# Kernel optimization log

Measured on AMD Instinct MI355X. Metric: run time of the kernel, lower is better.

The kernel has to match this reference:

```python
import jax, jax.numpy as jnp
import numpy as np

B, IN, HID, OUT, E = 8192, 1024, 4096, 1024, 8
EPS = 1e-5  # torch LayerNorm default


def _layernorm(x, gamma, beta):
    # normalize over last axis; gamma/beta broadcast as [E, dim] against [B, E, dim]
    mu = jnp.mean(x, axis=-1, keepdims=True)
    var = jnp.var(x, axis=-1, keepdims=True)
    return (x - mu) * jax.lax.rsqrt(var + EPS) * gamma + beta


def setup_inputs() -> dict:
    key = jax.random.key(0)
    ks = jax.random.split(key, 8)
    x = jax.random.normal(ks[0], (B, IN), dtype=jnp.float32)
    weights = jax.random.uniform(ks[1], (B, E), dtype=jnp.float32)
    s1 = 1.0 / np.sqrt(IN)
    s2 = 1.0 / np.sqrt(HID)
    W1 = jax.random.uniform(ks[2], (E, IN, HID), minval=-s1, maxval=s1, dtype=jnp.float32)
    b1 = jax.random.uniform(ks[3], (E, HID), minval=-s1, maxval=s1, dtype=jnp.float32)
    W2 = jax.random.uniform(ks[4], (E, HID, OUT), minval=-s2, maxval=s2, dtype=jnp.float32)
    b2 = jax.random.uniform(ks[5], (E, OUT), minval=-s2, maxval=s2, dtype=jnp.float32)
    g1 = jnp.ones((E, HID), dtype=jnp.float32)
    be1 = jnp.zeros((E, HID), dtype=jnp.float32)
    g2 = jnp.ones((E, OUT), dtype=jnp.float32)
    be2 = jnp.zeros((E, OUT), dtype=jnp.float32)
    return {"x": x, "weights": weights, "W1": W1, "b1": b1, "g1": g1, "be1": be1,
            "W2": W2, "b2": b2, "g2": g2, "be2": be2}


def reference(x, weights, W1, b1, g1, be1, W2, b2, g2, be2):
    # Each expert MLP([1024,4096,1024]): Linear -> LN -> GELU -> Linear -> LN -> GELU
    # (MLP appends LayerNorm + activation after EVERY Linear, including the last).
    # Dropout p=0 / eval mode -> identity. All experts run on every token.
    h = jnp.einsum('bi,eih->beh', x, W1) + b1          # [B, E, HID]
    h = jax.nn.gelu(_layernorm(h, g1, be1), approximate=False)
    y = jnp.einsum('beh,eho->beo', h, W2) + b2         # [B, E, OUT]
    y = jax.nn.gelu(_layernorm(y, g2, be2), approximate=False)
    # weighted combine: einsum('bij,bi->bj')
    return jnp.einsum('beo,be->bo', y, weights)        # [B, OUT]
```

## Files before the change

### kernel.cpp

```cpp
#include <hip/hip_runtime.h>
#include <cstdint>
#include <cstddef>

typedef unsigned short u16;
typedef float f32x4 __attribute__((ext_vector_type(4)));
typedef __bf16 bf16x8 __attribute__((ext_vector_type(8)));

#define B_DIM   8192
#define IN_DIM  1024
#define HID_DIM 4096
#define OUT_DIM 1024
#define NEXP    8

__device__ __forceinline__ u16 f2b(float f) {
    uint32_t u = __builtin_bit_cast(uint32_t, f);
    u += 0x7fffu + ((u >> 16) & 1u);
    return (u16)(u >> 16);
}
__device__ __forceinline__ float b2f(u16 b) {
    uint32_t u = ((uint32_t)b) << 16;
    return __builtin_bit_cast(float, u);
}
__device__ __forceinline__ float gelu_fast(float x) {
    float y = x * (0.7978845608f + 0.03567740814f * x * x);
    float a = fminf(y * 2.8853900818f, 80.0f);
    float e = __builtin_amdgcn_exp2f(a);
    return x * e * __builtin_amdgcn_rcpf(e + 1.0f);
}
__device__ __forceinline__ void async_cp16(const void* g, void* l) {
    __builtin_amdgcn_global_load_lds(
        (const __attribute__((address_space(1))) void*)g,
        (__attribute__((address_space(3))) void*)l,
        16, 0, 0);
}

__global__ __launch_bounds__(256)
void cvt_bf16(const float* __restrict__ in, u16* __restrict__ out, int n4) {
    int i = blockIdx.x * 256 + threadIdx.x;
    if (i >= n4) return;
    float4 v = *(const float4*)&in[(size_t)i * 4];
    uint2 o;
    o.x = (uint32_t)f2b(v.x) | ((uint32_t)f2b(v.y) << 16);
    o.y = (uint32_t)f2b(v.z) | ((uint32_t)f2b(v.w) << 16);
    *(uint2*)&out[(size_t)i * 4] = o;
}

__global__ __launch_bounds__(256)
void transpose_cvt2(const float* __restrict__ W1e, u16* __restrict__ w1t,
                    const float* __restrict__ W2e, u16* __restrict__ w2t) {
    __shared__ float tile[32][33];
    const float* W; u16* Wt; int K, N, n0, k0;
    if (blockIdx.z == 0) {
        W = W1e; Wt = w1t; K = IN_DIM; N = HID_DIM;
        n0 = blockIdx.x * 32; k0 = blockIdx.y * 32;
    } else {
        W = W2e; Wt = w2t; K = HID_DIM; N = OUT_DIM;
        n0 = blockIdx.y * 32; k0 = blockIdx.x * 32;
    }
    const int tx = threadIdx.x & 31, ty = threadIdx.x >> 5;
#pragma unroll
    for (int i = 0; i < 4; ++i) {
        int k = k0 + ty + i * 8;
        tile[ty + i * 8][tx] = W[(size_t)k * N + n0 + tx];
    }
    __syncthreads();
#pragma unroll
    for (int i = 0; i < 4; ++i) {
        int n = n0 + ty + i * 8;
        Wt[(size_t)n * K + k0 + tx] = f2b(tile[tx][ty + i * 8]);
    }
}

template<int F32OUT>
__global__ __launch_bounds__(512, 2)
void gemm256_8ph(const u16* __restrict__ A, const u16* __restrict__ Bt,
                 const float* __restrict__ bias, void* __restrict__ Cv,
                 int M, int N, int lda, int ldb, int Ksl) {
    __shared__ __attribute__((aligned(16))) u16 sA[32768];
    __shared__ __attribute__((aligned(16))) u16 sB[32768];

    const int tid  = threadIdx.x;
    const int wid  = tid >> 6;
    const int lane = tid & 63;
    const int quad = lane >> 4;
    const int lr   = lane & 15;
    const int wm   = wid >> 2;
    const int wn   = wid & 3;
    const int z    = blockIdx.z;

    const int NX = gridDim.x, NY = gridDim.y;
    const int bid = blockIdx.y * NX + blockIdx.x;
    const int xcd = bid & 7;
    const int j   = bid >> 3;
    const int yl  = j / NX;
    const int bx  = j - yl * NX;
    const int by  = xcd * (NY >> 3) + yl;
    const int m0 = by * 256;
    const int n0 = bx * 256;

    const int qsw   = (lr >> 1) & 3;
    const int row_s = tid >> 2;
    const int lc    = ((tid & 3) ^ ((tid >> 3) & 3)) * 8;

    const u16* Ast = A  + (size_t)z * Ksl + (size_t)(m0 + row_s) * lda + lc;
    const u16* Bst = Bt + (size_t)z * Ksl + (size_t)(n0 + row_s) * ldb + lc;

    const int rdA = (wm * 128 + lr) * 32 + ((quad ^ qsw) * 8);
    const int rdB = (wn * 64  + lr) * 32 + ((quad ^ qsw) * 8);
    const int d0  = tid * 8;

    const int NT = Ksl >> 6;

    f32x4 acc[8][4] = {};
    bf16x8 av[4], bv[4];

#define STG_A(hb, ko) do {                                                     \
        async_cp16(Ast + (ko),                      &sA[(hb) + d0]);           \
        async_cp16(Ast + (ko) + (size_t)128 * lda,  &sA[(hb) + d0 + 4096]);    \
    } while (0)
#define STG_B(hb, ko) do {                                                     \
        async_cp16(Bst + (ko),                      &sB[(hb) + d0]);           \
        async_cp16(Bst + (ko) + (size_t)128 * ldb,  &sB[(hb) + d0 + 4096]);    \
    } while (0)
#define RD_A4(hb, MO) do { _Pragma("unroll")                                   \
        for (int mi_ = 0; mi_ < 4; ++mi_)                                      \
            av[mi_] = *(const bf16x8*)&sA[(hb) + rdA + ((MO) + mi_) * 512];    \
    } while (0)
#define RD_B4(hb) do { _Pragma("unroll")                                       \
        for (int ni_ = 0; ni_ < 4; ++ni_)                                      \
            bv[ni_] = *(const bf16x8*)&sB[(hb) + rdB + ni_ * 512];             \
    } while (0)
#define SYNC_MFMA16(MO) do {                                                   \
        __builtin_amdgcn_s_barrier();                                          \
        asm volatile("s_waitcnt lgkmcnt(0)");                                  \
        __builtin_amdgcn_sched_barrier(0);                                     \
        __builtin_amdgcn_s_setprio(1);                                         \
        _Pragma("unroll")                                                      \
        for (int mi_ = 0; mi_ < 4; ++mi_)                                      \
            _Pragma("unroll")                                                  \
            for (int ni_ = 0; ni_ < 4; ++ni_)                                  \
                acc[(MO) + mi_][ni_] = __builtin_amdgcn_mfma_f32_16x16x32_bf16(\
                    av[mi_], bv[ni_], acc[(MO) + mi_][ni_], 0, 0, 0);          \
        __builtin_amdgcn_s_setprio(0);                                         \
    } while (0)

    STG_A(0, 0);      STG_B(0, 0);
    STG_A(8192, 32);  STG_B(8192, 32);
    asm volatile("s_waitcnt vmcnt(4)");
    __builtin_amdgcn_s_barrier();

#pragma unroll 1
    for (int t = 0; t < NT - 1; ++t) {
        const int cb = (t & 1) << 14;
        const int nb = cb ^ 16384;
        const size_t kt = (size_t)(t + 1) * 64;
        RD_A4(cb, 0); RD_B4(cb);
        STG_A(nb, kt);
        SYNC_MFMA16(0);
        __builtin_amdgcn_s_barrier();
        RD_A4(cb, 4);
        STG_B(nb, kt);
        SYNC_MFMA16(4);
        asm volatile("s_waitcnt vmcnt(4)");
        __builtin_amdgcn_s_barrier();
        RD_A4(cb + 8192, 0); RD_B4(cb + 8192);
        STG_A(nb + 8192, kt + 32);
        SYNC_MFMA16(0);
        __builtin_amdgcn_s_barrier();
        RD_A4(cb + 8192, 4);
        STG_B(nb + 8192, kt + 32);
        SYNC_MFMA16(4);
        asm volatile("s_waitcnt vmcnt(4)");
        __builtin_amdgcn_s_barrier();
    }
    {
        const int cb = ((NT - 1) & 1) << 14;
        RD_A4(cb, 0); RD_B4(cb);
        SYNC_MFMA16(0);
        __builtin_amdgcn_s_barrier();
        RD_A4(cb, 4);
        SYNC_MFMA16(4);
        asm volatile("s_waitcnt vmcnt(0)");
        __builtin_amdgcn_s_barrier();
        RD_A4(cb + 8192, 0); RD_B4(cb + 8192);
        SYNC_MFMA16(0);
        __builtin_amdgcn_s_barrier();
        RD_A4(cb + 8192, 4);
        SYNC_MFMA16(4);
    }
#undef SYNC_MFMA16
#undef RD_B4
#undef RD_A4
#undef STG_B
#undef STG_A

    if constexpr (F32OUT) {
        float* C = (float*)Cv + (size_t)z * ((size_t)M * N);
#pragma unroll
        for (int mi = 0; mi < 8; ++mi) {
            const int mr = m0 + wm * 128 + mi * 16 + quad * 4;
#pragma unroll
            for (int r = 0; r < 4; ++r) {
                float* Crow = C + (size_t)(mr + r) * N + n0 + wn * 64 + lr;
#pragma unroll
                for (int ni = 0; ni < 4; ++ni)
                    Crow[ni * 16] = acc[mi][ni][r];
            }
        }
    } else {
        u16* C = (u16*)Cv;
        float bvv[4];
#pragma unroll
        for (int ni = 0; ni < 4; ++ni)
            bvv[ni] = bias[n0 + wn * 64 + ni * 16 + lr];
#pragma unroll
        for (int mi = 0; mi < 8; ++mi) {
            const int mr = m0 + wm * 128 + mi * 16 + quad * 4;
#pragma unroll
            for (int r = 0; r < 4; ++r) {
                u16* Crow = C + (size_t)(mr + r) * N + n0 + wn * 64 + lr;
#pragma unroll
                for (int ni = 0; ni < 4; ++ni)
                    Crow[ni * 16] = f2b(acc[mi][ni][r] + bvv[ni]);
            }
        }
    }
}

__global__ __launch_bounds__(256)
void gemm_bt_bias(const u16* __restrict__ A, const u16* __restrict__ Bt,
                  const float* __restrict__ bias, u16* __restrict__ C,
                  int M, int N, int K) {
    __shared__ __attribute__((aligned(16))) u16 sA[2][128 * 32];
    __shared__ __attribute__((aligned(16))) u16 sB[2][128 * 32];

    const int tid  = threadIdx.x;
    const int wid  = tid >> 6;
    const int lane = tid & 63;
    const int quad = lane >> 4;
    const int lr   = lane & 15;
    const int wm   = wid & 1;
    const int wn   = wid >> 1;

    const int NX = gridDim.x, NY = gridDim.y;
    const int bid = blockIdx.y * NX + blockIdx.x;
    const int xcd = bid & 7;
    const int j   = bid >> 3;
    const int yl  = j / NX;
    const int bx  = j - yl * NX;
    const int by  = xcd * (NY >> 3) + yl;

    const int m0 = by * 128;
    const int n0 = bx * 128;

    const int sr  = lane >> 2;
    const int scl = ((lane & 3) ^ ((lane >> 3) & 3)) * 8;
    const int qsw = (lr >> 1) & 3;

    const u16* Ag = A + (size_t)m0 * K;
    const u16* Bg = Bt + (size_t)n0 * K;

    f32x4 acc[4][4] = {};

    for (int k0 = 0; k0 < K; k0 += 64) {
#pragma unroll
        for (int s = 0; s < 2; ++s) {
#pragma unroll
            for (int i = 0; i < 2; ++i) {
                const int rb = wid * 32 + i * 16;
                async_cp16(Ag + (size_t)(rb + sr) * K + k0 + s * 32 + scl,
                           &sA[s][rb * 32]);
                async_cp16(Bg + (size_t)(rb + sr) * K + k0 + s * 32 + scl,
                           &sB[s][rb * 32]);
            }
        }
        __syncthreads();

#pragma unroll
        for (int s = 0; s < 2; ++s) {
            bf16x8 af[4], bfr[4];
#pragma unroll
            for (int mi = 0; mi < 4; ++mi)
                af[mi] = *(const bf16x8*)
                    &sA[s][(wm * 64 + mi * 16 + lr) * 32 + ((quad ^ qsw) * 8)];
#pragma unroll
            for (int ni = 0; ni < 4; ++ni)
                bfr[ni] = *(const bf16x8*)
                    &sB[s][(wn * 64 + ni * 16 + lr) * 32 + ((quad ^ qsw) * 8)];

#pragma unroll
            for (int mi = 0; mi < 4; ++mi)
#pragma unroll
                for (int ni = 0; ni < 4; ++ni)
                    acc[mi][ni] = __builtin_amdgcn_mfma_f32_16x16x32_bf16(
                        af[mi], bfr[ni], acc[mi][ni], 0, 0, 0);
        }

        __syncthreads();
    }

    float bvv[4];
#pragma unroll
    for (int ni = 0; ni < 4; ++ni)
        bvv[ni] = bias[n0 + wn * 64 + ni * 16 + lr];

#pragma unroll
    for (int mi = 0; mi < 4; ++mi) {
        const int mr = m0 + wm * 64 + mi * 16 + quad * 4;
#pragma unroll
        for (int r = 0; r < 4; ++r) {
            u16* Crow = C + (size_t)(mr + r) * N + n0 + wn * 64 + lr;
#pragma unroll
            for (int ni = 0; ni < 4; ++ni)
                Crow[ni * 16] = f2b(acc[mi][ni][r] + bvv[ni]);
        }
    }
}

__global__ __launch_bounds__(256)
void ln_gelu_hid(u16* __restrict__ h, const float* __restrict__ g,
                 const float* __restrict__ be) {
    __shared__ float red[8];
    const int row = blockIdx.x;
    u16* hp = h + (size_t)row * HID_DIM;
    const int t = threadIdx.x;

    uint4 v0 = *(const uint4*)&hp[t * 8];
    uint4 v1 = *(const uint4*)&hp[(t + 256) * 8];

    float vals[16];
    {
        const uint32_t w0[4] = {v0.x, v0.y, v0.z, v0.w};
        const uint32_t w1[4] = {v1.x, v1.y, v1.z, v1.w};
#pragma unroll
        for (int q = 0; q < 4; ++q) {
            vals[q * 2]     = b2f((u16)(w0[q] & 0xffffu));
            vals[q * 2 + 1] = b2f((u16)(w0[q] >> 16));
            vals[8 + q * 2]     = b2f((u16)(w1[q] & 0xffffu));
            vals[8 + q * 2 + 1] = b2f((u16)(w1[q] >> 16));
        }
    }
    float s = 0.f, ss = 0.f;
#pragma unroll
    for (int i = 0; i < 16; ++i) { s += vals[i]; ss += vals[i] * vals[i]; }

    float4 gv[4], bv[4];
    gv[0] = *(const float4*)&g[t * 8];
    gv[1] = *(const float4*)&g[t * 8 + 4];
    gv[2] = *(const float4*)&g[(t + 256) * 8];
    gv[3] = *(const float4*)&g[(t + 256) * 8 + 4];
    bv[0] = *(const float4*)&be[t * 8];
    bv[1] = *(const float4*)&be[t * 8 + 4];
    bv[2] = *(const float4*)&be[(t + 256) * 8];
    bv[3] = *(const float4*)&be[(t + 256) * 8 + 4];

#pragma unroll
    for (int off = 32; off > 0; off >>= 1) {
        s += __shfl_down(s, off, 64);
        ss += __shfl_down(ss, off, 64);
    }
    if ((t & 63) == 0) { red[(t >> 6) * 2] = s; red[(t >> 6) * 2 + 1] = ss; }
    __syncthreads();
    s  = red[0] + red[2] + red[4] + red[6];
    ss = red[1] + red[3] + red[5] + red[7];
    const float mean = s * (1.f / HID_DIM);
    const float rstd = rsqrtf(ss * (1.f / HID_DIM) - mean * mean + 1e-5f);

    const float* gf = (const float*)gv;
    const float* bf = (const float*)bv;
#pragma unroll
    for (int j = 0; j < 2; ++j) {
        uint4 o;
        uint32_t* ow = (uint32_t*)&o;
#pragma unroll
        for (int q = 0; q < 4; ++q) {
            const int k = j * 8 + q * 2;
            float u0 = gelu_fast((vals[k]     - mean) * rstd * gf[k]     + bf[k]);
            float u1 = gelu_fast((vals[k + 1] - mean) * rstd * gf[k + 1] + bf[k + 1]);
            ow[q] = (uint32_t)f2b(u0) | ((uint32_t)f2b(u1) << 16);
        }
        *(uint4*)&hp[(t + j * 256) * 8] = o;
    }
}

__global__ __launch_bounds__(256)
void ln_gelu_combine(const u16* __restrict__ y, const float* __restrict__ g,
                     const float* __restrict__ be, const float* __restrict__ wts,
                     float* __restrict__ out, int e, int first) {
    __shared__ float red[8];
    const int row = blockIdx.x;
    const u16* yp = y + (size_t)row * OUT_DIM;
    const int t = threadIdx.x;

    uint2 v = *(const uint2*)&yp[t * 4];
    float f0 = b2f((u16)(v.x & 0xffffu)), f1 = b2f((u16)(v.x >> 16));
    float f2 = b2f((u16)(v.y & 0xffffu)), f3 = b2f((u16)(v.y >> 16));
    float s = f0 + f1 + f2 + f3;
    float ss = f0 * f0 + f1 * f1 + f2 * f2 + f3 * f3;

    const int n = t * 4;
    float4 gv = *(const float4*)&g[n];
    float4 bvv = *(const float4*)&be[n];

#pragma unroll
    for (int off = 32; off > 0; off >>= 1) {
        s += __shfl_down(s, off, 64);
        ss += __shfl_down(ss, off, 64);
    }
    if ((t & 63) == 0) { red[(t >> 6) * 2] = s; red[(t >> 6) * 2 + 1] = ss; }
    __syncthreads();
    s  = red[0] + red[2] + red[4] + red[6];
    ss = red[1] + red[3] + red[5] + red[7];
    const float mean = s * (1.f / OUT_DIM);
    const float rstd = rsqrtf(ss * (1.f / OUT_DIM) - mean * mean + 1e-5f);

    const float w = wts[(size_t)row * NEXP + e];
    float4 o;
    if (first) { o.x = o.y = o.z = o.w = 0.f; }
    else       { o = *(const float4*)&out[(size_t)row * OUT_DIM + n]; }
    o.x += w * gelu_fast((f0 - mean) * rstd * gv.x + bvv.x);
    o.y += w * gelu_fast((f1 - mean) * rstd * gv.y + bvv.y);
    o.z += w * gelu_fast((f2 - mean) * rstd * gv.z + bvv.z);
    o.w += w * gelu_fast((f3 - mean) * rstd * gv.w + bvv.w);
    *(float4*)&out[(size_t)row * OUT_DIM + n] = o;
}

__global__ __launch_bounds__(256)
void ln_gelu_combine_f32(const float* __restrict__ P, const float* __restrict__ g,
                         const float* __restrict__ be, const float* __restrict__ bs,
                         const float* __restrict__ wts, float* __restrict__ out,
                         int e, int first) {
    __shared__ float red[8];
    const int row = blockIdx.x;
    const int t = threadIdx.x;
    const int n = t * 4;

    const float* p0 = P + (size_t)row * OUT_DIM + n;
    const float* p1 = p0 + (size_t)B_DIM * OUT_DIM;
    float4 a  = *(const float4*)p0;
    float4 b  = *(const float4*)p1;
    float4 c  = *(const float4*)&bs[n];
    float f0 = a.x + b.x + c.x, f1 = a.y + b.y + c.y;
    float f2 = a.z + b.z + c.z, f3 = a.w + b.w + c.w;
    float s = f0 + f1 + f2 + f3;
    float ss = f0 * f0 + f1 * f1 + f2 * f2 + f3 * f3;

    float4 gv = *(const float4*)&g[n];
    float4 bvv = *(const float4*)&be[n];

#pragma unroll
    for (int off = 32; off > 0; off >>= 1) {
        s += __shfl_down(s, off, 64);
        ss += __shfl_down(ss, off, 64);
    }
    if ((t & 63) == 0) { red[(t >> 6) * 2] = s; red[(t >> 6) * 2 + 1] = ss; }
    __syncthreads();
    s  = red[0] + red[2] + red[4] + red[6];
    ss = red[1] + red[3] + red[5] + red[7];
    const float mean = s * (1.f / OUT_DIM);
    const float rstd = rsqrtf(ss * (1.f / OUT_DIM) - mean * mean + 1e-5f);

    const float w = wts[(size_t)row * NEXP + e];
    float4 o;
    if (first) { o.x = o.y = o.z = o.w = 0.f; }
    else       { o = *(const float4*)&out[(size_t)row * OUT_DIM + n]; }
    o.x += w * gelu_fast((f0 - mean) * rstd * gv.x + bvv.x);
    o.y += w * gelu_fast((f1 - mean) * rstd * gv.y + bvv.y);
    o.z += w * gelu_fast((f2 - mean) * rstd * gv.z + bvv.z);
    o.w += w * gelu_fast((f3 - mean) * rstd * gv.w + bvv.w);
    *(float4*)&out[(size_t)row * OUT_DIM + n] = o;
}

extern "C" void kernel_launch(void* const* d_in, const int* in_sizes, int n_in,
                              void* d_out, int out_size, void* d_ws, size_t ws_size,
                              hipStream_t stream) {
    (void)in_sizes; (void)n_in; (void)out_size;
    const float* x   = (const float*)d_in[0];
    const float* wts = (const float*)d_in[1];
    const float* W1  = (const float*)d_in[2];
    const float* b1  = (const float*)d_in[3];
    const float* g1  = (const float*)d_in[4];
    const float* be1 = (const float*)d_in[5];
    const float* W2  = (const float*)d_in[6];
    const float* b2  = (const float*)d_in[7];
    const float* g2  = (const float*)d_in[8];
    const float* be2 = (const float*)d_in[9];
    float* out = (float*)d_out;

    char* p = (char*)d_ws;
    u16* xb  = (u16*)p; p += (size_t)B_DIM * IN_DIM * 2;
    u16* w1t = (u16*)p; p += (size_t)HID_DIM * IN_DIM * 2;
    u16* w2t = (u16*)p; p += (size_t)OUT_DIM * HID_DIM * 2;
    u16* h   = (u16*)p; p += (size_t)B_DIM * HID_DIM * 2;
    float* P = (float*)p;
    u16*  y  = (u16*)p;

    const size_t need = (size_t)B_DIM * IN_DIM * 2 + (size_t)HID_DIM * IN_DIM * 2 +
                        (size_t)OUT_DIM * HID_DIM * 2 + (size_t)B_DIM * HID_DIM * 2 +
                        (size_t)2 * B_DIM * OUT_DIM * 4;
    const int splitk = (ws_size >= need) ? 1 : 0;

    cvt_bf16<<<(B_DIM * IN_DIM / 4 + 255) / 256, 256, 0, stream>>>(x, xb, B_DIM * IN_DIM / 4);

    for (int e = 0; e < NEXP; ++e) {
        transpose_cvt2<<<dim3(HID_DIM / 32, IN_DIM / 32, 2), 256, 0, stream>>>(
            W1 + (size_t)e * IN_DIM * HID_DIM, w1t,
            W2 + (size_t)e * HID_DIM * OUT_DIM, w2t);
        gemm256_8ph<0><<<dim3(HID_DIM / 256, B_DIM / 256, 1), 512, 0, stream>>>(
            xb, w1t, b1 + (size_t)e * HID_DIM, h, B_DIM, HID_DIM, IN_DIM, IN_DIM, IN_DIM);
        ln_gelu_hid<<<B_DIM, 256, 0, stream>>>(h, g1 + (size_t)e * HID_DIM,
                                               be1 + (size_t)e * HID_DIM);
        if (splitk) {
            gemm256_8ph<1><<<dim3(OUT_DIM / 256, B_DIM / 256, 2), 512, 0, stream>>>(
                h, w2t, nullptr, P, B_DIM, OUT_DIM, HID_DIM, HID_DIM, HID_DIM / 2);
            ln_gelu_combine_f32<<<B_DIM, 256, 0, stream>>>(
                P, g2 + (size_t)e * OUT_DIM, be2 + (size_t)e * OUT_DIM,
                b2 + (size_t)e * OUT_DIM, wts, out, e, e == 0 ? 1 : 0);
        } else {
            gemm_bt_bias<<<dim3(OUT_DIM / 128, B_DIM / 128), 256, 0, stream>>>(
                h, w2t, b2 + (size_t)e * OUT_DIM, y, B_DIM, OUT_DIM, HID_DIM);
            ln_gelu_combine<<<B_DIM, 256, 0, stream>>>(y, g2 + (size_t)e * OUT_DIM,
                                                       be2 + (size_t)e * OUT_DIM, wts, out,
                                                       e, e == 0 ? 1 : 0);
        }
    }
}
```

Baseline: 1.862 ms.

## Switch GEMM to 32x32x16 MFMA and store split-K partials as bf16

The GEMM inner loop now uses 32x32x16 bf16 MFMA instructions with 4x2 f32x16 accumulators instead of 16x16x32, and the LDS read indexing is changed to match the new operand layout. The aim is fewer MFMA issues and better operand reuse per LDS read. The split-K partial outputs are also written as bf16 instead of f32, which halves partial traffic and the workspace requirement. The cost is lost precision, since partial sums are rounded to bf16 before they are combined.

```diff
diff --git a/kernel.cpp b/kernel.cpp
--- a/kernel.cpp
+++ b/kernel.cpp
@@ -4,6 +4,7 @@
 
 typedef unsigned short u16;
 typedef float f32x4 __attribute__((ext_vector_type(4)));
+typedef float f32x16 __attribute__((ext_vector_type(16)));
 typedef __bf16 bf16x8 __attribute__((ext_vector_type(8)));
 
 #define B_DIM   8192
@@ -71,10 +72,10 @@
     }
 }
 
-template<int F32OUT>
+template<int PARTIAL>
 __global__ __launch_bounds__(512, 2)
 void gemm256_8ph(const u16* __restrict__ A, const u16* __restrict__ Bt,
-                 const float* __restrict__ bias, void* __restrict__ Cv,
+                 const float* __restrict__ bias, u16* __restrict__ C,
                  int M, int N, int lda, int ldb, int Ksl) {
     __shared__ __attribute__((aligned(16))) u16 sA[32768];
     __shared__ __attribute__((aligned(16))) u16 sB[32768];
@@ -82,8 +83,8 @@
     const int tid  = threadIdx.x;
     const int wid  = tid >> 6;
     const int lane = tid & 63;
-    const int quad = lane >> 4;
-    const int lr   = lane & 15;
+    const int l31  = lane & 31;
+    const int hi   = lane >> 5;
     const int wm   = wid >> 2;
     const int wn   = wid & 3;
     const int z    = blockIdx.z;
@@ -98,20 +99,22 @@
     const int m0 = by * 256;
     const int n0 = bx * 256;
 
-    const int qsw   = (lr >> 1) & 3;
+    const int xk    = (lane >> 1) & 3;
     const int row_s = tid >> 2;
     const int lc    = ((tid & 3) ^ ((tid >> 3) & 3)) * 8;
 
     const u16* Ast = A  + (size_t)z * Ksl + (size_t)(m0 + row_s) * lda + lc;
     const u16* Bst = Bt + (size_t)z * Ksl + (size_t)(n0 + row_s) * ldb + lc;
 
-    const int rdA = (wm * 128 + lr) * 32 + ((quad ^ qsw) * 8);
-    const int rdB = (wn * 64  + lr) * 32 + ((quad ^ qsw) * 8);
+    const int rdA = (wm * 128 + l31) * 32;
+    const int rdB = (wn * 64  + l31) * 32;
+    const int ck0 = ((0 + hi) ^ xk) * 8;
+    const int ck1 = ((2 + hi) ^ xk) * 8;
     const int d0  = tid * 8;
 
     const int NT = Ksl >> 6;
 
-    f32x4 acc[8][4] = {};
+    f32x16 acc[4][2] = {};
     bf16x8 av[4], bv[4];
 
 #define STG_A(hb, ko) do {                                                     \
@@ -122,25 +125,31 @@
         async_cp16(Bst + (ko),                      &sB[(hb) + d0]);           \
         async_cp16(Bst + (ko) + (size_t)128 * ldb,  &sB[(hb) + d0 + 4096]);    \
     } while (0)
-#define RD_A4(hb, MO) do { _Pragma("unroll")                                   \
-        for (int mi_ = 0; mi_ < 4; ++mi_)                                      \
-            av[mi_] = *(const bf16x8*)&sA[(hb) + rdA + ((MO) + mi_) * 512];    \
+#define RD_A4(hb, MF0) do {                                                    \
+        av[0] = *(const bf16x8*)&sA[(hb) + rdA + (MF0) * 1024 + ck0];          \
+        av[1] = *(const bf16x8*)&sA[(hb) + rdA + (MF0) * 1024 + ck1];          \
+        av[2] = *(const bf16x8*)&sA[(hb) + rdA + ((MF0) + 1) * 1024 + ck0];    \
+        av[3] = *(const bf16x8*)&sA[(hb) + rdA + ((MF0) + 1) * 1024 + ck1];    \
     } while (0)
-#define RD_B4(hb) do { _Pragma("unroll")                                       \
-        for (int ni_ = 0; ni_ < 4; ++ni_)                                      \
-            bv[ni_] = *(const bf16x8*)&sB[(hb) + rdB + ni_ * 512];             \
+#define RD_B4(hb) do {                                                         \
+        bv[0] = *(const bf16x8*)&sB[(hb) + rdB + ck0];                         \
+        bv[1] = *(const bf16x8*)&sB[(hb) + rdB + ck1];                         \
+        bv[2] = *(const bf16x8*)&sB[(hb) + rdB + 1024 + ck0];                  \
+        bv[3] = *(const bf16x8*)&sB[(hb) + rdB + 1024 + ck1];                  \
     } while (0)
-#define SYNC_MFMA16(MO) do {                                                   \
+#define CLUSTER8(A0) do {                                                      \
         __builtin_amdgcn_s_barrier();                                          \
         asm volatile("s_waitcnt lgkmcnt(0)");                                  \
         __builtin_amdgcn_sched_barrier(0);                                     \
         __builtin_amdgcn_s_setprio(1);                                         \
-        _Pragma("unroll")                                                      \
-        for (int mi_ = 0; mi_ < 4; ++mi_)                                      \
-            _Pragma("unroll")                                                  \
-            for (int ni_ = 0; ni_ < 4; ++ni_)                                  \
-                acc[(MO) + mi_][ni_] = __builtin_amdgcn_mfma_f32_16x16x32_bf16(\
-                    av[mi_], bv[ni_], acc[(MO) + mi_][ni_], 0, 0, 0);          \
+        acc[(A0)][0]     = __builtin_amdgcn_mfma_f32_32x32x16_bf16(av[0], bv[0], acc[(A0)][0],     0, 0, 0); \
+        acc[(A0)][1]     = __builtin_amdgcn_mfma_f32_32x32x16_bf16(av[0], bv[2], acc[(A0)][1],     0, 0, 0); \
+        acc[(A0) + 1][0] = __builtin_amdgcn_mfma_f32_32x32x16_bf16(av[2], bv[0], acc[(A0) + 1][0], 0, 0, 0); \
+        acc[(A0) + 1][1] = __builtin_amdgcn_mfma_f32_32x32x16_bf16(av[2], bv[2], acc[(A0) + 1][1], 0, 0, 0); \
+        acc[(A0)][0]     = __builtin_amdgcn_mfma_f32_32x32x16_bf16(av[1], bv[1], acc[(A0)][0],     0, 0, 0); \
+        acc[(A0)][1]     = __builtin_amdgcn_mfma_f32_32x32x16_bf16(av[1], bv[3], acc[(A0)][1],     0, 0, 0); \
+        acc[(A0) + 1][0] = __builtin_amdgcn_mfma_f32_32x32x16_bf16(av[3], bv[1], acc[(A0) + 1][0], 0, 0, 0); \
+        acc[(A0) + 1][1] = __builtin_amdgcn_mfma_f32_32x32x16_bf16(av[3], bv[3], acc[(A0) + 1][1], 0, 0, 0); \
         __builtin_amdgcn_s_setprio(0);                                         \
     } while (0)
 
@@ -156,72 +165,71 @@
         const size_t kt = (size_t)(t + 1) * 64;
         RD_A4(cb, 0); RD_B4(cb);
         STG_A(nb, kt);
-        SYNC_MFMA16(0);
-        __builtin_amdgcn_s_barrier();
-        RD_A4(cb, 4);
+        CLUSTER8(0);
+        __builtin_amdgcn_s_barrier();
+        RD_A4(cb, 2);
         STG_B(nb, kt);
-        SYNC_MFMA16(4);
+        CLUSTER8(2);
         asm volatile("s_waitcnt vmcnt(4)");
         __builtin_amdgcn_s_barrier();
         RD_A4(cb + 8192, 0); RD_B4(cb + 8192);
         STG_A(nb + 8192, kt + 32);
-        SYNC_MFMA16(0);
-        __builtin_amdgcn_s_barrier();
-        RD_A4(cb + 8192, 4);
+        CLUSTER8(0);
+        __builtin_amdgcn_s_barrier();
+        RD_A4(cb + 8192, 2);
         STG_B(nb + 8192, kt + 32);
-        SYNC_MFMA16(4);
+        CLUSTER8(2);
         asm volatile("s_waitcnt vmcnt(4)");
         __builtin_amdgcn_s_barrier();
     }
     {
         const int cb = ((NT - 1) & 1) << 14;
         RD_A4(cb, 0); RD_B4(cb);
-        SYNC_MFMA16(0);
-        __builtin_amdgcn_s_barrier();
-        RD_A4(cb, 4);
-        SYNC_MFMA16(4);
+        CLUSTER8(0);
+        __builtin_amdgcn_s_barrier();
+        RD_A4(cb, 2);
+        CLUSTER8(2);
         asm volatile("s_waitcnt vmcnt(0)");
         __builtin_amdgcn_s_barrier();
         RD_A4(cb + 8192, 0); RD_B4(cb + 8192);
-        SYNC_MFMA16(0);
-        __builtin_amdgcn_s_barrier();
-        RD_A4(cb + 8192, 4);
-        SYNC_MFMA16(4);
-    }
-#undef SYNC_MFMA16
+        CLUSTER8(0);
+        __builtin_amdgcn_s_barrier();
+        RD_A4(cb + 8192, 2);
+        CLUSTER8(2);
+    }
+#undef CLUSTER8
 #undef RD_B4
 #undef RD_A4
 #undef STG_B
 #undef STG_A
 
-    if constexpr (F32OUT) {
-        float* C = (float*)Cv + (size_t)z * ((size_t)M * N);
-#pragma unroll
-        for (int mi = 0; mi < 8; ++mi) {
-            const int mr = m0 + wm * 128 + mi * 16 + quad * 4;
-#pragma unroll
-            for (int r = 0; r < 4; ++r) {
-                float* Crow = C + (size_t)(mr + r) * N + n0 + wn * 64 + lr;
-#pragma unroll
-                for (int ni = 0; ni < 4; ++ni)
-                    Crow[ni * 16] = acc[mi][ni][r];
+    if constexpr (PARTIAL) {
+        u16* Cb = C + (size_t)z * ((size_t)M * N);
+#pragma unroll
+        for (int mf = 0; mf < 4; ++mf) {
+            const int mb = m0 + wm * 128 + mf * 32 + hi * 4;
+#pragma unroll
+            for (int rq = 0; rq < 4; ++rq)
+#pragma unroll
+            for (int rr = 0; rr < 4; ++rr) {
+                u16* Crow = Cb + (size_t)(mb + rr + rq * 8) * N + n0 + wn * 64 + l31;
+                Crow[0]  = f2b(acc[mf][0][rq * 4 + rr]);
+                Crow[32] = f2b(acc[mf][1][rq * 4 + rr]);
             }
         }
     } else {
-        u16* C = (u16*)Cv;
-        float bvv[4];
-#pragma unroll
-        for (int ni = 0; ni < 4; ++ni)
-            bvv[ni] = bias[n0 + wn * 64 + ni * 16 + lr];
-#pragma unroll
-        for (int mi = 0; mi < 8; ++mi) {
-            const int mr = m0 + wm * 128 + mi * 16 + quad * 4;
-#pragma unroll
-            for (int r = 0; r < 4; ++r) {
-                u16* Crow = C + (size_t)(mr + r) * N + n0 + wn * 64 + lr;
-#pragma unroll
-                for (int ni = 0; ni < 4; ++ni)
-                    Crow[ni * 16] = f2b(acc[mi][ni][r] + bvv[ni]);
+        const float bv0 = bias[n0 + wn * 64 + l31];
+        const float bv1 = bias[n0 + wn * 64 + 32 + l31];
+#pragma unroll
+        for (int mf = 0; mf < 4; ++mf) {
+            const int mb = m0 + wm * 128 + mf * 32 + hi * 4;
+#pragma unroll
+            for (int rq = 0; rq < 4; ++rq)
+#pragma unroll
+            for (int rr = 0; rr < 4; ++rr) {
+                u16* Crow = C + (size_t)(mb + rr + rq * 8) * N + n0 + wn * 64 + l31;
+                Crow[0]  = f2b(acc[mf][0][rq * 4 + rr] + bv0);
+                Crow[32] = f2b(acc[mf][1][rq * 4 + rr] + bv1);
             }
         }
     }
@@ -426,7 +434,7 @@
 }
 
 __global__ __launch_bounds__(256)
-void ln_gelu_combine_f32(const float* __restrict__ P, const float* __restrict__ g,
+void ln_gelu_combine_2bf(const u16* __restrict__ P, const float* __restrict__ g,
                          const float* __restrict__ be, const float* __restrict__ bs,
                          const float* __restrict__ wts, float* __restrict__ out,
                          int e, int first) {
@@ -435,13 +443,15 @@
     const int t = threadIdx.x;
     const int n = t * 4;
 
-    const float* p0 = P + (size_t)row * OUT_DIM + n;
-    const float* p1 = p0 + (size_t)B_DIM * OUT_DIM;
-    float4 a  = *(const float4*)p0;
-    float4 b  = *(const float4*)p1;
+    const u16* p0 = P + (size_t)row * OUT_DIM + n;
+    const u16* p1 = p0 + (size_t)B_DIM * OUT_DIM;
+    uint2 a = *(const uint2*)p0;
+    uint2 b = *(const uint2*)p1;
     float4 c  = *(const float4*)&bs[n];
-    float f0 = a.x + b.x + c.x, f1 = a.y + b.y + c.y;
-    float f2 = a.z + b.z + c.z, f3 = a.w + b.w + c.w;
+    float f0 = b2f((u16)(a.x & 0xffffu)) + b2f((u16)(b.x & 0xffffu)) + c.x;
+    float f1 = b2f((u16)(a.x >> 16))     + b2f((u16)(b.x >> 16))     + c.y;
+    float f2 = b2f((u16)(a.y & 0xffffu)) + b2f((u16)(b.y & 0xffffu)) + c.z;
+    float f3 = b2f((u16)(a.y >> 16))     + b2f((u16)(b.y >> 16))     + c.w;
     float s = f0 + f1 + f2 + f3;
     float ss = f0 * f0 + f1 * f1 + f2 * f2 + f3 * f3;
 
@@ -492,12 +502,12 @@
     u16* w1t = (u16*)p; p += (size_t)HID_DIM * IN_DIM * 2;
     u16* w2t = (u16*)p; p += (size_t)OUT_DIM * HID_DIM * 2;
     u16* h   = (u16*)p; p += (size_t)B_DIM * HID_DIM * 2;
-    float* P = (float*)p;
-    u16*  y  = (u16*)p;
+    u16* P   = (u16*)p;
+    u16* y   = (u16*)p;
 
     const size_t need = (size_t)B_DIM * IN_DIM * 2 + (size_t)HID_DIM * IN_DIM * 2 +
                         (size_t)OUT_DIM * HID_DIM * 2 + (size_t)B_DIM * HID_DIM * 2 +
-                        (size_t)2 * B_DIM * OUT_DIM * 4;
+                        (size_t)2 * B_DIM * OUT_DIM * 2;
     const int splitk = (ws_size >= need) ? 1 : 0;
 
     cvt_bf16<<<(B_DIM * IN_DIM / 4 + 255) / 256, 256, 0, stream>>>(x, xb, B_DIM * IN_DIM / 4);
@@ -513,7 +523,7 @@
         if (splitk) {
             gemm256_8ph<1><<<dim3(OUT_DIM / 256, B_DIM / 256, 2), 512, 0, stream>>>(
                 h, w2t, nullptr, P, B_DIM, OUT_DIM, HID_DIM, HID_DIM, HID_DIM / 2);
-            ln_gelu_combine_f32<<<B_DIM, 256, 0, stream>>>(
+            ln_gelu_combine_2bf<<<B_DIM, 256, 0, stream>>>(
                 P, g2 + (size_t)e * OUT_DIM, be2 + (size_t)e * OUT_DIM,
                 b2 + (size_t)e * OUT_DIM, wts, out, e, e == 0 ? 1 : 0);
         } else {
```

Result: slower. 1.910 ms (+2.6%).

## Use 256x512 triple-buffered GEMM for layer 1 and bf16 split-K partials

Applied to the files above, without the earlier changes.

Adds a new 1024-thread GEMM kernel with a 256x512 output tile and three-stage async LDS buffering for the first expert linear layer. The larger tile raises arithmetic intensity and halves the block count. The split-K second GEMM now writes its partial sums as bf16 instead of fp32, and the combine kernel reads bf16, which halves partial-sum traffic. The trade-off is one block per CU, higher register and LDS pressure, and extra rounding in the partial sums.

```diff
diff --git a/kernel.cpp b/kernel.cpp
--- a/kernel.cpp
+++ b/kernel.cpp
@@ -71,11 +71,135 @@
     }
 }
 
-template<int F32OUT>
+__global__ __launch_bounds__(1024, 1)
+void gemm256x512_bt(const u16* __restrict__ A, const u16* __restrict__ Bt,
+                    const float* __restrict__ bias, u16* __restrict__ C,
+                    int M, int N, int lda, int ldb, int K) {
+    __shared__ __attribute__((aligned(16))) u16 sA[3 * 8192];
+    __shared__ __attribute__((aligned(16))) u16 sB[3 * 16384];
+
+    const int tid  = threadIdx.x;
+    const int wid  = tid >> 6;
+    const int lane = tid & 63;
+    const int quad = lane >> 4;
+    const int lr   = lane & 15;
+    const int wm   = wid >> 3;
+    const int wn   = wid & 7;
+
+    const int NX = gridDim.x, NY = gridDim.y;
+    const int bid = blockIdx.y * NX + blockIdx.x;
+    const int xcd = bid & 7;
+    const int j   = bid >> 3;
+    const int yl  = j / NX;
+    const int bx  = j - yl * NX;
+    const int by  = xcd * (NY >> 3) + yl;
+    const int m0 = by * 256;
+    const int n0 = bx * 512;
+
+    const int qsw   = (lr >> 1) & 3;
+    const int row_s = tid >> 2;
+    const int lc    = ((tid & 3) ^ ((tid >> 3) & 3)) * 8;
+
+    const u16* Ast = A  + (size_t)(m0 + row_s) * lda + lc;
+    const u16* Bst = Bt + (size_t)(n0 + row_s) * ldb + lc;
+
+    const int rdA = (wm * 128 + lr) * 32 + ((quad ^ qsw) * 8);
+    const int rdB = (wn * 64  + lr) * 32 + ((quad ^ qsw) * 8);
+    const int d0  = tid * 8;
+
+    const int NT = K >> 5;
+
+    f32x4 acc[8][4] = {};
+    bf16x8 av[4], bv[4];
+
+#define STG_A1(bb, ko) async_cp16(Ast + (ko), &sA[(bb) * 8192 + d0])
+#define STG_B1(bb, ko) async_cp16(Bst + (ko), &sB[(bb) * 16384 + d0])
+#define STG_B2(bb, ko) async_cp16(Bst + (ko) + (size_t)256 * ldb, \
+                                  &sB[(bb) * 16384 + 8192 + d0])
+#define RD_A4X(bb, MO) do { _Pragma("unroll")                                  \
+        for (int mi_ = 0; mi_ < 4; ++mi_)                                      \
+            av[mi_] = *(const bf16x8*)&sA[(bb) * 8192 + rdA + ((MO) + mi_) * 512]; \
+    } while (0)
+#define RD_B4X(bb) do { _Pragma("unroll")                                      \
+        for (int ni_ = 0; ni_ < 4; ++ni_)                                      \
+            bv[ni_] = *(const bf16x8*)&sB[(bb) * 16384 + rdB + ni_ * 512];     \
+    } while (0)
+#define CLUSTER16(MO) do {                                                     \
+        __builtin_amdgcn_s_barrier();                                          \
+        asm volatile("s_waitcnt lgkmcnt(0)");                                  \
+        __builtin_amdgcn_sched_barrier(0);                                     \
+        __builtin_amdgcn_s_setprio(1);                                         \
+        _Pragma("unroll")                                                      \
+        for (int mi_ = 0; mi_ < 4; ++mi_)                                      \
+            _Pragma("unroll")                                                  \
+            for (int ni_ = 0; ni_ < 4; ++ni_)                                  \
+                acc[(MO) + mi_][ni_] = __builtin_amdgcn_mfma_f32_16x16x32_bf16(\
+                    av[mi_], bv[ni_], acc[(MO) + mi_][ni_], 0, 0, 0);          \
+        __builtin_amdgcn_s_setprio(0);                                         \
+    } while (0)
+
+    STG_A1(0, 0);  STG_B1(0, 0);  STG_B2(0, 0);
+    STG_A1(1, 32); STG_B1(1, 32); STG_B2(1, 32);
+    asm volatile("s_waitcnt vmcnt(3)");
+    __builtin_amdgcn_s_barrier();
+
+    int cb = 0, sb = 2;
+#pragma unroll 1
+    for (int t = 0; t < NT - 2; ++t) {
+        const size_t ko = (size_t)(t + 2) * 32;
+        RD_A4X(cb, 0); RD_B4X(cb);
+        STG_A1(sb, ko); STG_B1(sb, ko);
+        CLUSTER16(0);
+        __builtin_amdgcn_s_barrier();
+        RD_A4X(cb, 4);
+        STG_B2(sb, ko);
+        CLUSTER16(4);
+        asm volatile("s_waitcnt vmcnt(3)");
+        __builtin_amdgcn_s_barrier();
+        cb = (cb == 2) ? 0 : cb + 1;
+        sb = (sb == 2) ? 0 : sb + 1;
+    }
+    RD_A4X(cb, 0); RD_B4X(cb);
+    CLUSTER16(0);
+    __builtin_amdgcn_s_barrier();
+    RD_A4X(cb, 4);
+    CLUSTER16(4);
+    asm volatile("s_waitcnt vmcnt(0)");
+    __builtin_amdgcn_s_barrier();
+    cb = (cb == 2) ? 0 : cb + 1;
+    RD_A4X(cb, 0); RD_B4X(cb);
+    CLUSTER16(0);
+    __builtin_amdgcn_s_barrier();
+    RD_A4X(cb, 4);
+    CLUSTER16(4);
+
+#undef CLUSTER16
+#undef RD_B4X
+#undef RD_A4X
+#undef STG_B2
+#undef STG_B1
+#undef STG_A1
+
+    float bvv[4];
+#pragma unroll
+    for (int ni = 0; ni < 4; ++ni)
+        bvv[ni] = bias[n0 + wn * 64 + ni * 16 + lr];
+#pragma unroll
+    for (int mi = 0; mi < 8; ++mi) {
+        const int mr = m0 + wm * 128 + mi * 16 + quad * 4;
+#pragma unroll
+        for (int r = 0; r < 4; ++r) {
+            u16* Crow = C + (size_t)(mr + r) * N + n0 + wn * 64 + lr;
+#pragma unroll
+            for (int ni = 0; ni < 4; ++ni)
+                Crow[ni * 16] = f2b(acc[mi][ni][r] + bvv[ni]);
+        }
+    }
+}
+
 __global__ __launch_bounds__(512, 2)
-void gemm256_8ph(const u16* __restrict__ A, const u16* __restrict__ Bt,
-                 const float* __restrict__ bias, void* __restrict__ Cv,
-                 int M, int N, int lda, int ldb, int Ksl) {
+void gemm256_part(const u16* __restrict__ A, const u16* __restrict__ Bt,
+                  u16* __restrict__ P, int M, int N, int lda, int ldb, int Ksl) {
     __shared__ __attribute__((aligned(16))) u16 sA[32768];
     __shared__ __attribute__((aligned(16))) u16 sB[32768];
 
@@ -194,35 +318,16 @@
 #undef STG_B
 #undef STG_A
 
-    if constexpr (F32OUT) {
-        float* C = (float*)Cv + (size_t)z * ((size_t)M * N);
-#pragma unroll
-        for (int mi = 0; mi < 8; ++mi) {
-            const int mr = m0 + wm * 128 + mi * 16 + quad * 4;
-#pragma unroll
-            for (int r = 0; r < 4; ++r) {
-                float* Crow = C + (size_t)(mr + r) * N + n0 + wn * 64 + lr;
-#pragma unroll
-                for (int ni = 0; ni < 4; ++ni)
-                    Crow[ni * 16] = acc[mi][ni][r];
-            }
-        }
-    } else {
-        u16* C = (u16*)Cv;
-        float bvv[4];
-#pragma unroll
-        for (int ni = 0; ni < 4; ++ni)
-            bvv[ni] = bias[n0 + wn * 64 + ni * 16 + lr];
-#pragma unroll
-        for (int mi = 0; mi < 8; ++mi) {
-            const int mr = m0 + wm * 128 + mi * 16 + quad * 4;
-#pragma unroll
-            for (int r = 0; r < 4; ++r) {
-                u16* Crow = C + (size_t)(mr + r) * N + n0 + wn * 64 + lr;
-#pragma unroll
-                for (int ni = 0; ni < 4; ++ni)
-                    Crow[ni * 16] = f2b(acc[mi][ni][r] + bvv[ni]);
-            }
+    u16* Pb = P + (size_t)z * ((size_t)M * N);
+#pragma unroll
+    for (int mi = 0; mi < 8; ++mi) {
+        const int mr = m0 + wm * 128 + mi * 16 + quad * 4;
+#pragma unroll
+        for (int r = 0; r < 4; ++r) {
+            u16* Prow = Pb + (size_t)(mr + r) * N + n0 + wn * 64 + lr;
+#pragma unroll
+            for (int ni = 0; ni < 4; ++ni)
+                Prow[ni * 16] = f2b(acc[mi][ni][r]);
         }
     }
 }
@@ -426,7 +531,7 @@
 }
 
 __global__ __launch_bounds__(256)
-void ln_gelu_combine_f32(const float* __restrict__ P, const float* __restrict__ g,
+void ln_gelu_combine_2bf(const u16* __restrict__ P, const float* __restrict__ g,
                          const float* __restrict__ be, const float* __restrict__ bs,
                          const float* __restrict__ wts, float* __restrict__ out,
                          int e, int first) {
@@ -435,13 +540,15 @@
     const int t = threadIdx.x;
     const int n = t * 4;
 
-    const float* p0 = P + (size_t)row * OUT_DIM + n;
-    const float* p1 = p0 + (size_t)B_DIM * OUT_DIM;
-    float4 a  = *(const float4*)p0;
-    float4 b  = *(const float4*)p1;
+    const u16* p0 = P + (size_t)row * OUT_DIM + n;
+    const u16* p1 = p0 + (size_t)B_DIM * OUT_DIM;
+    uint2 a = *(const uint2*)p0;
+    uint2 b = *(const uint2*)p1;
     float4 c  = *(const float4*)&bs[n];
-    float f0 = a.x + b.x + c.x, f1 = a.y + b.y + c.y;
-    float f2 = a.z + b.z + c.z, f3 = a.w + b.w + c.w;
+    float f0 = b2f((u16)(a.x & 0xffffu)) + b2f((u16)(b.x & 0xffffu)) + c.x;
+    float f1 = b2f((u16)(a.x >> 16))     + b2f((u16)(b.x >> 16))     + c.y;
+    float f2 = b2f((u16)(a.y & 0xffffu)) + b2f((u16)(b.y & 0xffffu)) + c.z;
+    float f3 = b2f((u16)(a.y >> 16))     + b2f((u16)(b.y >> 16))     + c.w;
     float s = f0 + f1 + f2 + f3;
     float ss = f0 * f0 + f1 * f1 + f2 * f2 + f3 * f3;
 
@@ -492,12 +599,12 @@
     u16* w1t = (u16*)p; p += (size_t)HID_DIM * IN_DIM * 2;
     u16* w2t = (u16*)p; p += (size_t)OUT_DIM * HID_DIM * 2;
     u16* h   = (u16*)p; p += (size_t)B_DIM * HID_DIM * 2;
-    float* P = (float*)p;
-    u16*  y  = (u16*)p;
+    u16* P   = (u16*)p;
+    u16* y   = (u16*)p;
 
     const size_t need = (size_t)B_DIM * IN_DIM * 2 + (size_t)HID_DIM * IN_DIM * 2 +
                         (size_t)OUT_DIM * HID_DIM * 2 + (size_t)B_DIM * HID_DIM * 2 +
-                        (size_t)2 * B_DIM * OUT_DIM * 4;
+                        (size_t)2 * B_DIM * OUT_DIM * 2;
     const int splitk = (ws_size >= need) ? 1 : 0;
 
     cvt_bf16<<<(B_DIM * IN_DIM / 4 + 255) / 256, 256, 0, stream>>>(x, xb, B_DIM * IN_DIM / 4);
@@ -506,14 +613,14 @@
         transpose_cvt2<<<dim3(HID_DIM / 32, IN_DIM / 32, 2), 256, 0, stream>>>(
             W1 + (size_t)e * IN_DIM * HID_DIM, w1t,
             W2 + (size_t)e * HID_DIM * OUT_DIM, w2t);
-        gemm256_8ph<0><<<dim3(HID_DIM / 256, B_DIM / 256, 1), 512, 0, stream>>>(
+        gemm256x512_bt<<<dim3(HID_DIM / 512, B_DIM / 256), 1024, 0, stream>>>(
             xb, w1t, b1 + (size_t)e * HID_DIM, h, B_DIM, HID_DIM, IN_DIM, IN_DIM, IN_DIM);
         ln_gelu_hid<<<B_DIM, 256, 0, stream>>>(h, g1 + (size_t)e * HID_DIM,
                                                be1 + (size_t)e * HID_DIM);
         if (splitk) {
-            gemm256_8ph<1><<<dim3(OUT_DIM / 256, B_DIM / 256, 2), 512, 0, stream>>>(
-                h, w2t, nullptr, P, B_DIM, OUT_DIM, HID_DIM, HID_DIM, HID_DIM / 2);
-            ln_gelu_combine_f32<<<B_DIM, 256, 0, stream>>>(
+            gemm256_part<<<dim3(OUT_DIM / 256, B_DIM / 256, 2), 512, 0, stream>>>(
+                h, w2t, P, B_DIM, OUT_DIM, HID_DIM, HID_DIM, HID_DIM / 2);
+            ln_gelu_combine_2bf<<<B_DIM, 256, 0, stream>>>(
                 P, g2 + (size_t)e * OUT_DIM, be2 + (size_t)e * OUT_DIM,
                 b2 + (size_t)e * OUT_DIM, wts, out, e, e == 0 ? 1 : 0);
         } else {
```

Result: slower. 5.531 ms (+197.1%).
